# Kernel optimization log

Measured on AMD Instinct MI355X. Metric: run time of the kernel, lower is better.

The kernel has to match this reference:

```python
import math
import jax, jax.numpy as jnp
import numpy as np

B, S, D, H = 2, 2048, 1024, 16
DH = D // H
DFF = 4 * D
EPS = 1e-6
MASKED_BIAS = -10000.0


def _gelu(x):
    # GPT-2 tanh-approx GELU
    return 0.5 * x * (1.0 + jnp.tanh(math.sqrt(2.0 / math.pi) * (x + 0.044715 * x ** 3)))


def _layernorm(x, w, b):
    mean = jnp.mean(x, axis=-1, keepdims=True)
    var = jnp.mean((x - mean) ** 2, axis=-1, keepdims=True)
    return w * ((x - mean) / jnp.sqrt(var + EPS)) + b


def setup_inputs() -> dict:
    key = jax.random.key(0)
    ks = jax.random.split(key, 6)
    std = 0.02
    return {
        "hidden_states": jax.random.normal(ks[0], (B, S, D), jnp.float32),
        "w_attn": jax.random.normal(ks[1], (D, 3 * D), jnp.float32) * std,
        "b_attn": jnp.zeros((3 * D,), jnp.float32),
        "w_proj": jax.random.normal(ks[2], (D, D), jnp.float32) * std,
        "b_proj": jnp.zeros((D,), jnp.float32),
        "w_fc": jax.random.normal(ks[3], (D, DFF), jnp.float32) * std,
        "b_fc": jnp.zeros((DFF,), jnp.float32),
        "w_fc_proj": jax.random.normal(ks[4], (DFF, D), jnp.float32) * std,
        "b_fc_proj": jnp.zeros((D,), jnp.float32),
        "ln1_w": jnp.ones((D,), jnp.float32),
        "ln1_b": jnp.zeros((D,), jnp.float32),
        "ln2_w": jnp.ones((D,), jnp.float32),
        "ln2_b": jnp.zeros((D,), jnp.float32),
    }


def reference(hidden_states, w_attn, b_attn, w_proj, b_proj, w_fc, b_fc,
              w_fc_proj, b_fc_proj, ln1_w, ln1_b, ln2_w, ln2_b):
    residual = hidden_states
    x = _layernorm(hidden_states, ln1_w, ln1_b)

    # c_attn: [B,S,D] @ [D,3D] + b -> split into q,k,v
    qkv = x @ w_attn + b_attn
    q, k, v = jnp.split(qkv, 3, axis=-1)
    # split heads -> [B,H,S,DH]
    q = q.reshape(B, S, H, DH).transpose(0, 2, 1, 3)
    k = k.reshape(B, S, H, DH).transpose(0, 2, 1, 3)
    v = v.reshape(B, S, H, DH).transpose(0, 2, 1, 3)

    scores = jnp.einsum('bhqd,bhkd->bhqk', q, k) / jnp.sqrt(jnp.float32(DH))
    causal = jnp.tril(jnp.ones((S, S), bool))  # [S,S]
    scores = jnp.where(causal[None, None], scores, jnp.float32(MASKED_BIAS))
    attn = jax.nn.softmax(scores, axis=-1)
    out = jnp.einsum('bhqk,bhkd->bhqd', attn, v)
    out = out.transpose(0, 2, 1, 3).reshape(B, S, D)
    out = out @ w_proj + b_proj

    h = residual + out
    residual = h
    y = _layernorm(h, ln2_w, ln2_b)
    y = _gelu(y @ w_fc + b_fc)
    y = y @ w_fc_proj + b_fc_proj
    return residual + y
```

## Files before the change

kernel.cpp:

```cpp
#include <hip/hip_runtime.h>
#include <cstdint>
#include <cstddef>

typedef unsigned short u16;
typedef float  floatx4 __attribute__((ext_vector_type(4)));
typedef short  short8  __attribute__((ext_vector_type(8)));
typedef u16    usx4    __attribute__((ext_vector_type(4)));
typedef u16    usx8    __attribute__((ext_vector_type(8)));

__device__ __forceinline__ u16 f2b(float f) {
  unsigned u = __float_as_uint(f);
  unsigned r = u + 0x7fffu + ((u >> 16) & 1u);
  return (u16)(r >> 16);
}
__device__ __forceinline__ float b2f(u16 s) {
  return __uint_as_float(((unsigned)s) << 16);
}

__device__ __forceinline__ float gelu_f(float x) {
  const float c = 0.7978845608028654f;
  float t = tanhf(c * (x + 0.044715f * x * x * x));
  return 0.5f * x * (1.0f + t);
}

__device__ __forceinline__ void gl2lds16(const u16* g, u16* l) {
  __builtin_amdgcn_global_load_lds(
      (const __attribute__((address_space(1))) unsigned int*)g,
      (__attribute__((address_space(3))) unsigned int*)l, 16, 0, 0);
}

#define C2SCALE 0.18033688011112042f

__global__ __launch_bounds__(256) void ln_bf16_kernel(
    const float* __restrict__ in, const float* __restrict__ w,
    const float* __restrict__ b, u16* __restrict__ out)
{
  const int row = blockIdx.x;
  const int t = threadIdx.x;
  const float* p = in + (size_t)row * 1024 + t * 4;
  floatx4 v = *(const floatx4*)p;
  float s  = v.x + v.y + v.z + v.w;
  float ss = v.x*v.x + v.y*v.y + v.z*v.z + v.w*v.w;
  #pragma unroll
  for (int m = 1; m < 64; m <<= 1) {
    s  += __shfl_xor(s,  m);
    ss += __shfl_xor(ss, m);
  }
  __shared__ float red[8];
  if ((t & 63) == 0) { red[(t >> 6)*2] = s; red[(t >> 6)*2 + 1] = ss; }
  __syncthreads();
  s  = red[0] + red[2] + red[4] + red[6];
  ss = red[1] + red[3] + red[5] + red[7];
  const float mean = s * (1.0f / 1024.0f);
  const float var  = ss * (1.0f / 1024.0f) - mean * mean;
  const float rstd = rsqrtf(var + 1e-6f);
  floatx4 wv = *(const floatx4*)(w + t * 4);
  floatx4 bv = *(const floatx4*)(b + t * 4);
  usx4 o = { f2b(wv.x * ((v.x - mean) * rstd) + bv.x),
             f2b(wv.y * ((v.y - mean) * rstd) + bv.y),
             f2b(wv.z * ((v.z - mean) * rstd) + bv.z),
             f2b(wv.w * ((v.w - mean) * rstd) + bv.w) };
  *(usx4*)(out + (size_t)row * 1024 + t * 4) = o;
}

__global__ __launch_bounds__(256) void wtrans_kernel(
    const float* __restrict__ in, u16* __restrict__ out, int K, int N)
{
  __shared__ u16 tile[32][33];
  const int n0 = blockIdx.x * 32, k0 = blockIdx.y * 32;
  const int tx = threadIdx.x & 31, ty = threadIdx.x >> 5;
  #pragma unroll
  for (int i = 0; i < 4; ++i)
    tile[ty + i*8][tx] = f2b(in[(size_t)(k0 + ty + i*8) * N + n0 + tx]);
  __syncthreads();
  #pragma unroll
  for (int i = 0; i < 4; ++i)
    out[(size_t)(n0 + ty + i*8) * K + k0 + tx] = tile[tx][ty + i*8];
}

template<int BM, int BN, int FLAGS, int MINW>
__global__ __launch_bounds__(256, MINW) void gemm_mfma_kernel(
    const u16* __restrict__ A, const u16* __restrict__ Bt,
    const float* __restrict__ bias, const float* __restrict__ Res,
    void* __restrict__ Cout, int M, int N, int K, int kLen)
{
  constexpr int WM = BM / 2, WN = BN / 2;
  constexpr int MT = WM / 16, NT = WN / 16;
  __shared__ u16 As[BM * 32];
  __shared__ u16 Bs[BN * 32];

  const int t = threadIdx.x;
  const int wave = t >> 6, lane = t & 63;
  const int quad = lane >> 4, l16 = lane & 15;
  const int wm = wave >> 1, wn = wave & 1;
  const int bm0 = blockIdx.y * BM, bn0 = blockIdx.x * BN;
  const int kStart = blockIdx.z * kLen;

  const int sRow = lane >> 2;
  const int sq   = lane & 3;

  const u16* aG[BM / 64];
  u16* aL[BM / 64];
  #pragma unroll
  for (int j = 0; j < BM / 64; ++j) {
    const int band = j * 4 + wave;
    aG[j] = A + (size_t)(bm0 + band * 16 + sRow) * K + kStart + sq * 8;
    aL[j] = As + band * 512;
  }
  const u16* bG[BN / 64];
  u16* bL[BN / 64];
  #pragma unroll
  for (int j = 0; j < BN / 64; ++j) {
    const int band = j * 4 + wave;
    bG[j] = Bt + (size_t)(bn0 + band * 16 + sRow) * K + kStart + sq * 8;
    bL[j] = Bs + band * 512;
  }

  floatx4 acc[MT][NT] = {};

  for (int k0 = 0; k0 < kLen; k0 += 32) {
    __syncthreads();
    #pragma unroll
    for (int j = 0; j < BM / 64; ++j) gl2lds16(aG[j] + k0, aL[j]);
    #pragma unroll
    for (int j = 0; j < BN / 64; ++j) gl2lds16(bG[j] + k0, bL[j]);
    __syncthreads();

    short8 af[MT], bf[NT];
    #pragma unroll
    for (int mt = 0; mt < MT; ++mt)
      af[mt] = *(const short8*)&As[(wm*WM + mt*16 + l16) * 32 + quad * 8];
    #pragma unroll
    for (int nt = 0; nt < NT; ++nt)
      bf[nt] = *(const short8*)&Bs[(wn*WN + nt*16 + l16) * 32 + quad * 8];
    #pragma unroll
    for (int mt = 0; mt < MT; ++mt)
      #pragma unroll
      for (int nt = 0; nt < NT; ++nt)
        acc[mt][nt] = __builtin_amdgcn_mfma_f32_16x16x32_bf16(af[mt], bf[nt], acc[mt][nt], 0, 0, 0);
  }

  const int orow0 = bm0 + wm * WM;
  const int ocol0 = bn0 + wn * WN;
  const size_t zoff = (size_t)blockIdx.z * M * N;
  #pragma unroll
  for (int nt = 0; nt < NT; ++nt) {
    const int col = ocol0 + nt*16 + l16;
    const float bv = bias ? bias[col] : 0.0f;
    const float postscale = ((FLAGS & 8) && col < 1024) ? C2SCALE : 1.0f;
    #pragma unroll
    for (int mt = 0; mt < MT; ++mt) {
      #pragma unroll
      for (int r = 0; r < 4; ++r) {
        const int row = orow0 + mt*16 + quad*4 + r;
        float v = acc[mt][nt][r] + bv;
        if (FLAGS & 1) v = gelu_f(v);
        if (FLAGS & 8) v *= postscale;
        if (FLAGS & 2) v += Res[(size_t)row * N + col];
        if (FLAGS & 4) ((u16*)Cout)[zoff + (size_t)row * N + col] = f2b(v);
        else           ((float*)Cout)[zoff + (size_t)row * N + col] = v;
      }
    }
  }
}

__global__ __launch_bounds__(256, 4) void attn_mfma_kernel(
    const u16* __restrict__ qkv, u16* __restrict__ opart, float* __restrict__ ml)
{
  __shared__ u16 Ks[64][72];
  __shared__ u16 Vt[64][72];
  __shared__ u16 Ps[64][72];

  const int t    = threadIdx.x;
  const int wave = t >> 6;
  const int lane = t & 63;
  const int quad = lane >> 4;
  const int l16  = lane & 15;
  const int pair = blockIdx.x >> 1;
  const int half = blockIdx.x & 1;
  const int h    = blockIdx.y;
  const int b    = blockIdx.z;

  const size_t base = (size_t)b * 2048 * 3072;
  const int qoff = h * 64;
  const int koff = 1024 + h * 64;
  const int voff = 2048 + h * 64;

  const int srow = t >> 2;
  const int scol = (t & 3) * 16;
  const int kpair  = t & 31;
  const int vchunk = t >> 5;

  const size_t obase  = ((((size_t)half * 2 + b) * 16 + h) * 2048) * 64;
  const size_t mlbase = ((((size_t)half * 2 + b) * 16 + h) * 2048) * 2;

  short8 onesb;
  {
    const short v = (l16 == 0) ? (short)0x3F80 : (short)0;
    #pragma unroll
    for (int i = 0; i < 8; ++i) onesb[i] = v;
  }

  #pragma unroll 1
  for (int iter = 0; iter < 2; ++iter) {
    const int qi = iter ? (31 - pair) : pair;
    const int q0 = qi << 6;
    const int T  = qi + 1;
    const int mid = (T + 1) >> 1;
    const int t0 = half ? mid : 0;
    const int t1 = half ? T : mid;

    floatx4 of[4] = {};
    floatx4 ofl = {};
    float m[4];
    #pragma unroll
    for (int r = 0; r < 4; ++r) m[r] = -1e30f;

    if (t0 < t1) {
      __syncthreads();
      {
        const u16* qp = qkv + base + (size_t)(q0 + srow) * 3072 + qoff + scol;
        *(usx8*)&Ks[srow][scol]     = *(const usx8*)qp;
        *(usx8*)&Ks[srow][scol + 8] = *(const usx8*)(qp + 8);
      }
      __syncthreads();
      const short8 qf0 = *(const short8*)&Ks[wave*16 + l16][quad*8];
      const short8 qf1 = *(const short8*)&Ks[wave*16 + l16][32 + quad*8];

      usx8 kr0, kr1, vr0, vr1;
      {
        const int k0 = t0 << 6;
        const u16* kp = qkv + base + (size_t)(k0 + srow) * 3072 + koff + scol;
        kr0 = *(const usx8*)kp; kr1 = *(const usx8*)(kp + 8);
        const u16* vp = qkv + base + (size_t)(k0 + 2*kpair) * 3072 + voff + vchunk*8;
        vr0 = *(const usx8*)vp; vr1 = *(const usx8*)(vp + 3072);
      }

      for (int tIdx = t0; tIdx < t1; ++tIdx) {
        __syncthreads();
        *(usx8*)&Ks[srow][scol]     = kr0;
        *(usx8*)&Ks[srow][scol + 8] = kr1;
        #pragma unroll
        for (int i = 0; i < 8; ++i)
          *(unsigned*)&Vt[vchunk*8 + i][2*kpair] =
              (unsigned)vr0[i] | ((unsigned)vr1[i] << 16);
        __syncthreads();

        if (tIdx + 1 < t1) {
          const int kn = (tIdx + 1) << 6;
          const u16* kp = qkv + base + (size_t)(kn + srow) * 3072 + koff + scol;
          kr0 = *(const usx8*)kp; kr1 = *(const usx8*)(kp + 8);
          const u16* vp = qkv + base + (size_t)(kn + 2*kpair) * 3072 + voff + vchunk*8;
          vr0 = *(const usx8*)vp; vr1 = *(const usx8*)(vp + 3072);
        }

        const int k0 = tIdx << 6;
        floatx4 sf[4];
        #pragma unroll
        for (int kt = 0; kt < 4; ++kt) {
          short8 kf0 = *(const short8*)&Ks[kt*16 + l16][quad*8];
          short8 kf1 = *(const short8*)&Ks[kt*16 + l16][32 + quad*8];
          floatx4 z = {};
          z      = __builtin_amdgcn_mfma_f32_16x16x32_bf16(qf0, kf0, z, 0, 0, 0);
          sf[kt] = __builtin_amdgcn_mfma_f32_16x16x32_bf16(qf1, kf1, z, 0, 0, 0);
        }

        const bool diag = (tIdx == qi);
        #pragma unroll
        for (int r = 0; r < 4; ++r) {
          float sv0 = sf[0][r], sv1 = sf[1][r], sv2 = sf[2][r], sv3 = sf[3][r];
          if (diag) {
            const int qrow = q0 + wave*16 + quad*4 + r;
            if (k0 +      l16 > qrow) sv0 = -1e30f;
            if (k0 + 16 + l16 > qrow) sv1 = -1e30f;
            if (k0 + 32 + l16 > qrow) sv2 = -1e30f;
            if (k0 + 48 + l16 > qrow) sv3 = -1e30f;
          }
          float mx = fmaxf(fmaxf(sv0, sv1), fmaxf(sv2, sv3));
          #pragma unroll
          for (int msk = 1; msk < 16; msk <<= 1) mx = fmaxf(mx, __shfl_xor(mx, msk, 16));
          const float nm = fmaxf(m[r], mx);
          const float alpha = exp2f(m[r] - nm);
          m[r] = nm;
          Ps[wave*16 + quad*4 + r][     l16] = f2b(exp2f(sv0 - nm));
          Ps[wave*16 + quad*4 + r][16 + l16] = f2b(exp2f(sv1 - nm));
          Ps[wave*16 + quad*4 + r][32 + l16] = f2b(exp2f(sv2 - nm));
          Ps[wave*16 + quad*4 + r][48 + l16] = f2b(exp2f(sv3 - nm));
          #pragma unroll
          for (int dht = 0; dht < 4; ++dht) of[dht][r] *= alpha;
          ofl[r] *= alpha;
        }

        short8 pf0 = *(const short8*)&Ps[wave*16 + l16][quad*8];
        short8 pf1 = *(const short8*)&Ps[wave*16 + l16][32 + quad*8];
        #pragma unroll
        for (int dht = 0; dht < 4; ++dht) {
          short8 vf0 = *(const short8*)&Vt[dht*16 + l16][quad*8];
          short8 vf1 = *(const short8*)&Vt[dht*16 + l16][32 + quad*8];
          of[dht] = __builtin_amdgcn_mfma_f32_16x16x32_bf16(pf0, vf0, of[dht], 0, 0, 0);
          of[dht] = __builtin_amdgcn_mfma_f32_16x16x32_bf16(pf1, vf1, of[dht], 0, 0, 0);
        }
        ofl = __builtin_amdgcn_mfma_f32_16x16x32_bf16(pf0, onesb, ofl, 0, 0, 0);
        ofl = __builtin_amdgcn_mfma_f32_16x16x32_bf16(pf1, onesb, ofl, 0, 0, 0);
      }
    }

    #pragma unroll
    for (int r = 0; r < 4; ++r) {
      const int s = q0 + wave*16 + quad*4 + r;
      u16* orow = opart + obase + (size_t)s * 64;
      #pragma unroll
      for (int dht = 0; dht < 4; ++dht) orow[dht*16 + l16] = f2b(of[dht][r]);
      const float lr = __shfl(ofl[r], quad * 16);
      if (l16 == 0) { ml[mlbase + 2*s] = m[r]; ml[mlbase + 2*s + 1] = lr; }
    }
  }
}

__global__ __launch_bounds__(256) void attn_combine_kernel(
    const u16* __restrict__ opart, const float* __restrict__ ml,
    u16* __restrict__ out)
{
  const int t = threadIdx.x;
  const int s = blockIdx.x * 4 + (t >> 6);
  const int lane = t & 63;
  const int h = blockIdx.y, b = blockIdx.z;

  const size_t o0  = ((((size_t)0 * 2 + b) * 16 + h) * 2048 + s) * 64 + lane;
  const size_t o1  = ((((size_t)1 * 2 + b) * 16 + h) * 2048 + s) * 64 + lane;
  const size_t ml0 = ((((size_t)0 * 2 + b) * 16 + h) * 2048 + s) * 2;
  const size_t ml1 = ((((size_t)1 * 2 + b) * 16 + h) * 2048 + s) * 2;

  const float m0 = ml[ml0], l0 = ml[ml0 + 1];
  const float m1 = ml[ml1], l1 = ml[ml1 + 1];
  const float M  = fmaxf(m0, m1);
  const float w0 = exp2f(m0 - M), w1 = exp2f(m1 - M);
  const float L  = w0 * l0 + w1 * l1;
  const float o  = w0 * b2f(opart[o0]) + w1 * b2f(opart[o1]);
  out[((size_t)b * 2048 + s) * 1024 + h * 64 + lane] = f2b(o / L);
}

__global__ __launch_bounds__(256) void fcproj_combine_kernel(
    const u16* __restrict__ p, const float* __restrict__ res,
    const float* __restrict__ bias, float* __restrict__ out)
{
  const size_t i0 = ((size_t)blockIdx.x * 256 + threadIdx.x) * 8;
  usx8 a = *(const usx8*)(p + i0);
  usx8 c = *(const usx8*)(p + 4194304 + i0);
  const int col = (int)(i0 & 1023);
  floatx4 bv0 = *(const floatx4*)(bias + col);
  floatx4 bv1 = *(const floatx4*)(bias + col + 4);
  floatx4 h0 = *(const floatx4*)(res + i0);
  floatx4 h1 = *(const floatx4*)(res + i0 + 4);
  floatx4 o0, o1;
  #pragma unroll
  for (int i = 0; i < 4; ++i) o0[i] = h0[i] + b2f(a[i])   + b2f(c[i])   + bv0[i];
  #pragma unroll
  for (int i = 0; i < 4; ++i) o1[i] = h1[i] + b2f(a[4+i]) + b2f(c[4+i]) + bv1[i];
  *(floatx4*)(out + i0)     = o0;
  *(floatx4*)(out + i0 + 4) = o1;
}

extern "C" void kernel_launch(void* const* d_in, const int* in_sizes, int n_in,
                              void* d_out, int out_size, void* d_ws, size_t ws_size,
                              hipStream_t stream) {
  const float* hidden    = (const float*)d_in[0];
  const float* w_attn    = (const float*)d_in[1];
  const float* b_attn    = (const float*)d_in[2];
  const float* w_proj    = (const float*)d_in[3];
  const float* b_proj    = (const float*)d_in[4];
  const float* w_fc      = (const float*)d_in[5];
  const float* b_fc      = (const float*)d_in[6];
  const float* w_fc_proj = (const float*)d_in[7];
  const float* b_fc_proj = (const float*)d_in[8];
  const float* ln1_w     = (const float*)d_in[9];
  const float* ln1_b     = (const float*)d_in[10];
  const float* ln2_w     = (const float*)d_in[11];
  const float* ln2_b     = (const float*)d_in[12];

  char* wsb = (char*)d_ws;
  u16*   xb    = (u16*)  (wsb + (size_t)( 0u << 20));
  u16*   qkvb  = (u16*)  (wsb + (size_t)( 8u << 20));
  u16*   attnb = (u16*)  (wsb + (size_t)(32u << 20));
  float* hbuf  = (float*)(wsb + (size_t)(40u << 20));
  u16*   opart = (u16*)  (wsb + (size_t)(40u << 20));
  float* mlbuf = (float*)(wsb + (size_t)(56u << 20));
  u16*   wqT   = (u16*)  (wsb + (size_t)(56u << 20));
  u16*   wpT   = (u16*)  (wsb + (size_t)(62u << 20));
  u16*   wfT   = (u16*)  (wsb + (size_t)(64u << 20));
  u16*   wfpT  = (u16*)  (wsb + (size_t)(72u << 20));
  u16*   pfcp  = (u16*)  (wsb + (size_t)(56u << 20));
  u16*   fcb   = qkvb;
  u16*   yb    = xb;

  wtrans_kernel<<<dim3(96, 32),  256, 0, stream>>>(w_attn,    wqT,  1024, 3072);
  wtrans_kernel<<<dim3(32, 32),  256, 0, stream>>>(w_proj,    wpT,  1024, 1024);
  wtrans_kernel<<<dim3(128, 32), 256, 0, stream>>>(w_fc,      wfT,  1024, 4096);
  wtrans_kernel<<<dim3(32, 128), 256, 0, stream>>>(w_fc_proj, wfpT, 4096, 1024);

  ln_bf16_kernel<<<4096, 256, 0, stream>>>(hidden, ln1_w, ln1_b, xb);
  gemm_mfma_kernel<128,128,12,4><<<dim3(24, 32, 1), 256, 0, stream>>>(
      xb, wqT, b_attn, nullptr, qkvb, 4096, 3072, 1024, 1024);
  attn_mfma_kernel<<<dim3(32, 16, 2), 256, 0, stream>>>(qkvb, opart, mlbuf);
  attn_combine_kernel<<<dim3(512, 16, 2), 256, 0, stream>>>(opart, mlbuf, attnb);
  gemm_mfma_kernel<128,64,2,4><<<dim3(16, 32, 1), 256, 0, stream>>>(
      attnb, wpT, b_proj, hidden, hbuf, 4096, 1024, 1024, 1024);
  ln_bf16_kernel<<<4096, 256, 0, stream>>>(hbuf, ln2_w, ln2_b, yb);
  gemm_mfma_kernel<256,128,5,2><<<dim3(32, 16, 1), 256, 0, stream>>>(
      yb, wfT, b_fc, nullptr, fcb, 4096, 4096, 1024, 1024);
  gemm_mfma_kernel<128,128,4,4><<<dim3(8, 32, 2), 256, 0, stream>>>(
      fcb, wfpT, nullptr, nullptr, pfcp, 4096, 1024, 4096, 2048);
  fcproj_combine_kernel<<<dim3(2048), 256, 0, stream>>>(pfcp, hbuf, b_fc_proj, (float*)d_out);
}
```

Baseline: 386.7 us.

## Swizzle LDS tiles, cheaper GELU, split-K out-proj, retile FC GEMMs

Adds an XOR swizzle to the LDS layout of the MFMA GEMM to reduce bank conflicts on fragment reads. Replaces tanh-based GELU with an equivalent sigmoid form using hardware exp2 and reciprocal. Splits the attention output projection along K with a separate combine kernel, retiles the FC and FC-proj GEMMs for more blocks, and reorganizes the workspace layout. Extra combine pass and bf16 partials add traffic and rounding error in exchange for more parallelism.

```diff
diff --git a/kernel.cpp b/kernel.cpp
--- a/kernel.cpp
+++ b/kernel.cpp
@@ -18,9 +18,10 @@
 }
 
 __device__ __forceinline__ float gelu_f(float x) {
-  const float c = 0.7978845608028654f;
-  float t = tanhf(c * (x + 0.044715f * x * x * x));
-  return 0.5f * x * (1.0f + t);
+  const float k = 2.3022082f;
+  float u = x * (1.0f + 0.044715f * x * x);
+  float t = __builtin_amdgcn_exp2f(-k * u);
+  return x * __builtin_amdgcn_rcpf(1.0f + t);
 }
 
 __device__ __forceinline__ void gl2lds16(const u16* g, u16* l) {
@@ -82,7 +83,7 @@
 __global__ __launch_bounds__(256, MINW) void gemm_mfma_kernel(
     const u16* __restrict__ A, const u16* __restrict__ Bt,
     const float* __restrict__ bias, const float* __restrict__ Res,
-    void* __restrict__ Cout, int M, int N, int K, int kLen)
+    void* __restrict__ Cout, int M, int N, int K, int kLen, size_t zStride)
 {
   constexpr int WM = BM / 2, WN = BN / 2;
   constexpr int MT = WM / 16, NT = WN / 16;
@@ -97,7 +98,7 @@
   const int kStart = blockIdx.z * kLen;
 
   const int sRow = lane >> 2;
-  const int sq   = lane & 3;
+  const int sq   = (lane & 3) ^ (sRow & 3);
 
   const u16* aG[BM / 64];
   u16* aL[BM / 64];
@@ -117,6 +118,7 @@
   }
 
   floatx4 acc[MT][NT] = {};
+  const int rcol = (quad ^ (l16 & 3)) << 3;
 
   for (int k0 = 0; k0 < kLen; k0 += 32) {
     __syncthreads();
@@ -129,10 +131,10 @@
     short8 af[MT], bf[NT];
     #pragma unroll
     for (int mt = 0; mt < MT; ++mt)
-      af[mt] = *(const short8*)&As[(wm*WM + mt*16 + l16) * 32 + quad * 8];
+      af[mt] = *(const short8*)&As[(wm*WM + mt*16 + l16) * 32 + rcol];
     #pragma unroll
     for (int nt = 0; nt < NT; ++nt)
-      bf[nt] = *(const short8*)&Bs[(wn*WN + nt*16 + l16) * 32 + quad * 8];
+      bf[nt] = *(const short8*)&Bs[(wn*WN + nt*16 + l16) * 32 + rcol];
     #pragma unroll
     for (int mt = 0; mt < MT; ++mt)
       #pragma unroll
@@ -142,7 +144,7 @@
 
   const int orow0 = bm0 + wm * WM;
   const int ocol0 = bn0 + wn * WN;
-  const size_t zoff = (size_t)blockIdx.z * M * N;
+  const size_t zoff = (size_t)blockIdx.z * zStride;
   #pragma unroll
   for (int nt = 0; nt < NT; ++nt) {
     const int col = ocol0 + nt*16 + l16;
@@ -340,13 +342,14 @@
   out[((size_t)b * 2048 + s) * 1024 + h * 64 + lane] = f2b(o / L);
 }
 
-__global__ __launch_bounds__(256) void fcproj_combine_kernel(
-    const u16* __restrict__ p, const float* __restrict__ res,
-    const float* __restrict__ bias, float* __restrict__ out)
+__global__ __launch_bounds__(256) void ksplit_combine_kernel(
+    const u16* __restrict__ p0, const u16* __restrict__ p1,
+    const float* __restrict__ res, const float* __restrict__ bias,
+    float* __restrict__ out)
 {
   const size_t i0 = ((size_t)blockIdx.x * 256 + threadIdx.x) * 8;
-  usx8 a = *(const usx8*)(p + i0);
-  usx8 c = *(const usx8*)(p + 4194304 + i0);
+  usx8 a = *(const usx8*)(p0 + i0);
+  usx8 c = *(const usx8*)(p1 + i0);
   const int col = (int)(i0 & 1023);
   floatx4 bv0 = *(const floatx4*)(bias + col);
   floatx4 bv1 = *(const floatx4*)(bias + col + 4);
@@ -379,19 +382,22 @@
   const float* ln2_b     = (const float*)d_in[12];
 
   char* wsb = (char*)d_ws;
-  u16*   xb    = (u16*)  (wsb + (size_t)( 0u << 20));
-  u16*   qkvb  = (u16*)  (wsb + (size_t)( 8u << 20));
-  u16*   attnb = (u16*)  (wsb + (size_t)(32u << 20));
-  float* hbuf  = (float*)(wsb + (size_t)(40u << 20));
-  u16*   opart = (u16*)  (wsb + (size_t)(40u << 20));
-  float* mlbuf = (float*)(wsb + (size_t)(56u << 20));
-  u16*   wqT   = (u16*)  (wsb + (size_t)(56u << 20));
-  u16*   wpT   = (u16*)  (wsb + (size_t)(62u << 20));
-  u16*   wfT   = (u16*)  (wsb + (size_t)(64u << 20));
-  u16*   wfpT  = (u16*)  (wsb + (size_t)(72u << 20));
-  u16*   pfcp  = (u16*)  (wsb + (size_t)(56u << 20));
-  u16*   fcb   = qkvb;
-  u16*   yb    = xb;
+  u16*   qkvb  = (u16*)  (wsb + (size_t)( 0u << 20));
+  u16*   xb    = (u16*)  (wsb + (size_t)(24u << 20));
+  u16*   opart = (u16*)  (wsb + (size_t)(24u << 20));
+  float* mlbuf = (float*)(wsb + (size_t)(40u << 20));
+  u16*   attnb = (u16*)  (wsb + (size_t)(42u << 20));
+  u16*   wqT   = (u16*)  (wsb + (size_t)(50u << 20));
+  u16*   wpT   = (u16*)  (wsb + (size_t)(56u << 20));
+  u16*   wfT   = (u16*)  (wsb + (size_t)(58u << 20));
+  u16*   wfpT  = (u16*)  (wsb + (size_t)(66u << 20));
+  u16*   pproj = (u16*)  (wsb + (size_t)(24u << 20));
+  float* hbuf  = (float*)(wsb + (size_t)(42u << 20));
+  u16*   yb    = (u16*)  (wsb + (size_t)( 0u << 20));
+  u16*   fcb   = (u16*)  (wsb + (size_t)( 8u << 20));
+  u16*   pfcp0 = (u16*)  (wsb + (size_t)( 0u << 20));
+  u16*   pfcp1 = (u16*)  (wsb + (size_t)(58u << 20));
+  const size_t zstr_fcp = ((size_t)58u << 20) / 2;
 
   wtrans_kernel<<<dim3(96, 32),  256, 0, stream>>>(w_attn,    wqT,  1024, 3072);
   wtrans_kernel<<<dim3(32, 32),  256, 0, stream>>>(w_proj,    wpT,  1024, 1024);
@@ -400,15 +406,18 @@
 
   ln_bf16_kernel<<<4096, 256, 0, stream>>>(hidden, ln1_w, ln1_b, xb);
   gemm_mfma_kernel<128,128,12,4><<<dim3(24, 32, 1), 256, 0, stream>>>(
-      xb, wqT, b_attn, nullptr, qkvb, 4096, 3072, 1024, 1024);
+      xb, wqT, b_attn, nullptr, qkvb, 4096, 3072, 1024, 1024, 0);
   attn_mfma_kernel<<<dim3(32, 16, 2), 256, 0, stream>>>(qkvb, opart, mlbuf);
   attn_combine_kernel<<<dim3(512, 16, 2), 256, 0, stream>>>(opart, mlbuf, attnb);
-  gemm_mfma_kernel<128,64,2,4><<<dim3(16, 32, 1), 256, 0, stream>>>(
-      attnb, wpT, b_proj, hidden, hbuf, 4096, 1024, 1024, 1024);
+  gemm_mfma_kernel<128,64,4,4><<<dim3(16, 32, 2), 256, 0, stream>>>(
+      attnb, wpT, nullptr, nullptr, pproj, 4096, 1024, 1024, 512, 4194304);
+  ksplit_combine_kernel<<<dim3(2048), 256, 0, stream>>>(
+      pproj, pproj + 4194304, hidden, b_proj, hbuf);
   ln_bf16_kernel<<<4096, 256, 0, stream>>>(hbuf, ln2_w, ln2_b, yb);
-  gemm_mfma_kernel<256,128,5,2><<<dim3(32, 16, 1), 256, 0, stream>>>(
-      yb, wfT, b_fc, nullptr, fcb, 4096, 4096, 1024, 1024);
-  gemm_mfma_kernel<128,128,4,4><<<dim3(8, 32, 2), 256, 0, stream>>>(
-      fcb, wfpT, nullptr, nullptr, pfcp, 4096, 1024, 4096, 2048);
-  fcproj_combine_kernel<<<dim3(2048), 256, 0, stream>>>(pfcp, hbuf, b_fc_proj, (float*)d_out);
-}
+  gemm_mfma_kernel<128,128,5,4><<<dim3(32, 32, 1), 256, 0, stream>>>(
+      yb, wfT, b_fc, nullptr, fcb, 4096, 4096, 1024, 1024, 0);
+  gemm_mfma_kernel<128,64,4,4><<<dim3(16, 32, 2), 256, 0, stream>>>(
+      fcb, wfpT, nullptr, nullptr, pfcp0, 4096, 1024, 4096, 2048, zstr_fcp);
+  ksplit_combine_kernel<<<dim3(2048), 256, 0, stream>>>(
+      pfcp0, pfcp1, hbuf, b_fc_proj, (float*)d_out);
+}
```

Result: no change. 382.2 us (-1.1%).
